# Kernel tuning notes

Hardware: AMD Instinct MI355X
Metric: run time of the kernel (lower is better)

The kernel has to match this reference:

```python
import jax, jax.numpy as jnp
import numpy as np

B, DIM, L, H, W = 4, 128, 256, 8, 8
N = L * H * W
D_INNER, D_STATE, D_CONV, DT_RANK = 128, 8, 4, 8


def _ln(x, w, b, eps=1e-5):
    m = x.mean(-1, keepdims=True)
    v = ((x - m) ** 2).mean(-1, keepdims=True)
    return (x - m) * jax.lax.rsqrt(v + eps) * w + b


def _mamba_fusion(x, z_in, p, i):
    # x, z_in: (B, N, DIM). x drives the SSM; z_in provides the cross-modal gate.
    u = x @ p['Wx'][i]                                    # (B, N, D_INNER)
    z = z_in @ p['Wz'][i]                                 # (B, N, D_INNER)
    # causal depthwise conv1d along tokens, kernel D_CONV (torch pad=k-1 then truncate)
    up = jnp.pad(u, ((0, 0), (D_CONV - 1, 0), (0, 0)))
    w = p['conv_w'][i]                                    # (D_INNER, D_CONV)
    uc = sum(up[:, k:k + u.shape[1], :] * w[:, k] for k in range(D_CONV)) + p['conv_b'][i]
    uc = jax.nn.silu(uc)
    x_dbl = uc @ p['Wxproj'][i]                           # (B, N, DT_RANK + 2*D_STATE)
    dt_r, Bm, Cm = jnp.split(x_dbl, [DT_RANK, DT_RANK + D_STATE], axis=-1)
    dt = jax.nn.softplus(dt_r @ p['Wdt'][i] + p['bdt'][i])  # (B, N, D_INNER)
    A = -jnp.exp(p['A_log'][i])                           # (D_INNER, D_STATE)
    dA = jnp.exp(dt[..., None] * A)                       # (B, N, D_INNER, D_STATE)
    dBu = dt[..., None] * Bm[:, :, None, :] * uc[..., None]

    def step(h, inp):
        dA_t, dBu_t, C_t = inp
        h = dA_t * h + dBu_t                              # (B, D_INNER, D_STATE)
        return h, jnp.einsum('bds,bs->bd', h, C_t)

    h0 = jnp.zeros((u.shape[0], D_INNER, D_STATE), u.dtype)
    _, ys = jax.lax.scan(step, h0, (dA.swapaxes(0, 1), dBu.swapaxes(0, 1), Cm.swapaxes(0, 1)))
    y = ys.swapaxes(0, 1) + p['Dp'][i] * uc
    y = y * jax.nn.silu(z)
    return y @ p['Wout_m'][i] + p['bout_m'][i]


def _cross_block(in0, in1, p, i):
    skip = in0
    a = _ln(in0, p['ln0_w'][i], p['ln0_b'][i])
    b = _ln(in1, p['ln1_w'][i], p['ln1_b'][i])
    return skip + _mamba_fusion(a, b, p, i)


def setup_inputs() -> dict:
    key = jax.random.key(0)
    ks = jax.random.split(key, 16)
    s_in = 1.0 / np.sqrt(DIM)
    s_di = 1.0 / np.sqrt(D_INNER)
    inp = {
        'front': jax.random.normal(ks[0], (B, DIM, L, H, W), jnp.float32),
        'back': jax.random.normal(ks[1], (B, DIM, L, H, W), jnp.float32),
        'ln0_w': jnp.ones((2, DIM), jnp.float32),
        'ln0_b': jnp.zeros((2, DIM), jnp.float32),
        'ln1_w': jnp.ones((2, DIM), jnp.float32),
        'ln1_b': jnp.zeros((2, DIM), jnp.float32),
        'Wx': jax.random.normal(ks[2], (2, DIM, D_INNER), jnp.float32) * s_in,
        'Wz': jax.random.normal(ks[3], (2, DIM, D_INNER), jnp.float32) * s_in,
        'conv_w': jax.random.normal(ks[4], (2, D_INNER, D_CONV), jnp.float32) * 0.5,
        'conv_b': jnp.zeros((2, D_INNER), jnp.float32),
        'Wxproj': jax.random.normal(ks[5], (2, D_INNER, DT_RANK + 2 * D_STATE), jnp.float32) * s_di,
        'Wdt': jax.random.normal(ks[6], (2, DT_RANK, D_INNER), jnp.float32) * (1.0 / np.sqrt(DT_RANK)),
        'bdt': jnp.full((2, D_INNER), -4.6, jnp.float32),  # softplus^-1(~0.01)
        'A_log': jnp.broadcast_to(jnp.log(jnp.arange(1, D_STATE + 1, dtype=jnp.float32)), (2, D_INNER, D_STATE)).copy(),
        'Dp': jnp.ones((2, D_INNER), jnp.float32),
        'Wout_m': jax.random.normal(ks[7], (2, D_INNER, DIM), jnp.float32) * s_di,
        'bout_m': jnp.zeros((2, DIM), jnp.float32),
        'Wout': jax.random.normal(ks[8], (DIM, DIM), jnp.float32) * s_in,
        'bout': jnp.zeros((DIM,), jnp.float32),
    }
    return inp


def reference(front, back, ln0_w, ln0_b, ln1_w, ln1_b, Wx, Wz, conv_w, conv_b,
              Wxproj, Wdt, bdt, A_log, Dp, Wout_m, bout_m, Wout, bout):
    p = dict(ln0_w=ln0_w, ln0_b=ln0_b, ln1_w=ln1_w, ln1_b=ln1_b, Wx=Wx, Wz=Wz,
             conv_w=conv_w, conv_b=conv_b, Wxproj=Wxproj, Wdt=Wdt, bdt=bdt,
             A_log=A_log, Dp=Dp, Wout_m=Wout_m, bout_m=bout_m)
    ff = front.reshape(B, DIM, N).swapaxes(1, 2)          # (B, N, DIM)
    bf = back.reshape(B, DIM, N).swapaxes(1, 2)
    f_fus = _cross_block(ff, bf, p, 0)
    b_fus = _cross_block(bf, ff, p, 1)
    fusion = ((f_fus + b_fus) * 0.5) @ Wout + bout
    return fusion.swapaxes(1, 2).reshape(B, DIM, L, H, W)
```

## Files before the change

### kernel.cpp

```cpp
#include <hip/hip_runtime.h>

#define DEV static __device__ __forceinline__

typedef short s16x8 __attribute__((ext_vector_type(8)));
typedef float f32x4 __attribute__((ext_vector_type(4)));
typedef unsigned short u16;

DEV float b2f(u16 u){ return __uint_as_float(((unsigned int)u) << 16); }
DEV u16 f2b(float f){
  unsigned int x = __float_as_uint(f);
  x += 0x7fffu + ((x >> 16) & 1u);
  return (u16)(x >> 16);
}
DEV float silu_f(float x){ return x * __builtin_amdgcn_rcpf(1.f + __expf(-x)); }
DEV float softplus_f(float x){ return (x > 15.f) ? x : __logf(1.f + __expf(x)); }
DEV bool detf32(const void* lnw){ return *(const unsigned int*)lnw == 0x3F800000u; }
DEV float ldin(const void* p, long long i, bool f){
  return f ? ((const float*)p)[i] : b2f(((const u16*)p)[i]);
}

static constexpr int BATCH = 4;
static constexpr int NSEQ  = 16384;
static constexpr int RTOT  = BATCH * NSEQ;
static constexpr int GCH   = 256;
static constexpr int DIRSZ = BATCH*GCH*128*8;

DEV int swz(int row, int col){ return (row << 7) + (col ^ ((row & 7) << 3)); }

__global__ __launch_bounds__(256) void k_setup(
                        const void* ln0w, const void* ln0b, const void* ln1w, const void* ln1b,
                        const void* Wx, const void* Wz, const void* Wxp, const void* Wdt,
                        const void* bdt, const void* Alog, const void* convw, const void* convb,
                        const void* Dpr, const void* Woutm, const void* boutm,
                        const void* Wout, const void* bout,
                        u16* Wuz, u16* WdtBC, u16* Wcat, u16* WoutT,
                        float* buz, float* bdtf, float* bcat, float* boutf,
                        float* Aexp, float* convwF, float* convbF, float* DpF)
{
  bool f = detf32(ln0w);
  int tid = blockIdx.x * 256 + threadIdx.x;
  int gs  = gridDim.x * 256;
  for (int idx = tid; idx < 2*256*128; idx += gs){
    int d = idx >> 15; int n = (idx >> 7) & 255; int k = idx & 127;
    float wv;
    if (n < 128) wv = ldin(ln0w, d*128+k, f) * ldin(Wx, (long long)(d*128+k)*128 + n, f);
    else         wv = ldin(ln1w, (1-d)*128+k, f) * ldin(Wz, (long long)((1-d)*128+k)*128 + (n-128), f);
    Wuz[idx] = f2b(wv);
  }
  for (int idx = tid; idx < 2*256; idx += gs){
    int d = idx >> 8; int n = idx & 255;
    float s = 0.f;
    if (n < 128){
      for (int k = 0; k < 128; ++k)
        s += ldin(ln0b, d*128+k, f) * ldin(Wx, (long long)(d*128+k)*128 + n, f);
    } else {
      for (int k = 0; k < 128; ++k)
        s += ldin(ln1b, (1-d)*128+k, f) * ldin(Wz, (long long)((1-d)*128+k)*128 + (n-128), f);
    }
    buz[idx] = s;
  }
  for (int idx = tid; idx < 2*128; idx += gs)
    bdtf[idx] = ldin(bdt, idx, f);
  for (int idx = tid; idx < 2*144*128; idx += gs){
    int i = idx / (144*128); int rem = idx % (144*128); int n = rem >> 7; int k = rem & 127;
    if (n < 128){
      float s = 0.f;
      for (int j = 0; j < 8; ++j)
        s += ldin(Wxp, (long long)(i*128+k)*24 + j, f) * ldin(Wdt, (long long)(i*8+j)*128 + n, f);
      WdtBC[idx] = f2b(s);
    } else {
      WdtBC[idx] = f2b(ldin(Wxp, (long long)(i*128+k)*24 + (n - 120), f));
    }
  }
  for (int idx = tid; idx < 128*256; idx += gs){
    int n = idx >> 8; int k = idx & 255;
    Wcat[idx] = f2b(ldin(Woutm, (long long)k*128 + n, f));
  }
  for (int idx = tid; idx < 128*128; idx += gs){
    int n = idx >> 7, k = idx & 127;
    WoutT[idx] = f2b(ldin(Wout, (long long)k*128 + n, f));
  }
  for (int idx = tid; idx < 128; idx += gs){
    bcat[idx]  = ldin(boutm, idx, f) + ldin(boutm, 128 + idx, f);
    boutf[idx] = ldin(bout, idx, f);
  }
  for (int idx = tid; idx < 2*128*8; idx += gs)
    Aexp[idx] = -expf(ldin(Alog, idx, f));
  for (int idx = tid; idx < 2*128*4; idx += gs)
    convwF[idx] = ldin(convw, idx, f);
  for (int idx = tid; idx < 2*128; idx += gs){
    convbF[idx] = ldin(convb, idx, f);
    DpF[idx]   = ldin(Dpr, idx, f);
  }
}

__global__ __launch_bounds__(256) void k_ln(const void* front, const void* back, const void* ln0w,
                                            u16* xf, u16* xb, u16* sfbh)
{
  bool fF = detf32(ln0w);
  __shared__ u16 Af[64][130];
  __shared__ u16 Ab[64][130];
  __shared__ float Mf[64], Rf[64], Mb[64], Rb[64];
  int tid = threadIdx.x;
  long long r0 = (long long)blockIdx.x * 64;
  int b  = (int)(r0 >> 14);
  int n0 = (int)(r0 & 16383);
  if (fF){
    const float* fp = (const float*)front;
    const float* bp = (const float*)back;
    for (int it = 0; it < 8; ++it){
      int d = it*16 + (tid >> 4);
      int t = (tid & 15) * 4;
      long long gi = ((long long)(b*128 + d))*NSEQ + n0 + t;
      float4 vf = *(const float4*)&fp[gi];
      float4 vb = *(const float4*)&bp[gi];
      Af[t+0][d] = f2b(vf.x); Af[t+1][d] = f2b(vf.y);
      Af[t+2][d] = f2b(vf.z); Af[t+3][d] = f2b(vf.w);
      Ab[t+0][d] = f2b(vb.x); Ab[t+1][d] = f2b(vb.y);
      Ab[t+2][d] = f2b(vb.z); Ab[t+3][d] = f2b(vb.w);
    }
  } else {
    const u16* fp = (const u16*)front;
    const u16* bp = (const u16*)back;
    for (int it = 0; it < 4; ++it){
      int d = it*32 + (tid >> 3);
      int t = (tid & 7) * 8;
      long long gi = ((long long)(b*128 + d))*NSEQ + n0 + t;
      uint4 vf = *(const uint4*)&fp[gi];
      uint4 vb = *(const uint4*)&bp[gi];
      Af[t+0][d] = (u16)vf.x; Af[t+1][d] = (u16)(vf.x>>16);
      Af[t+2][d] = (u16)vf.y; Af[t+3][d] = (u16)(vf.y>>16);
      Af[t+4][d] = (u16)vf.z; Af[t+5][d] = (u16)(vf.z>>16);
      Af[t+6][d] = (u16)vf.w; Af[t+7][d] = (u16)(vf.w>>16);
      Ab[t+0][d] = (u16)vb.x; Ab[t+1][d] = (u16)(vb.x>>16);
      Ab[t+2][d] = (u16)vb.y; Ab[t+3][d] = (u16)(vb.y>>16);
      Ab[t+4][d] = (u16)vb.z; Ab[t+5][d] = (u16)(vb.z>>16);
      Ab[t+6][d] = (u16)vb.w; Ab[t+7][d] = (u16)(vb.w>>16);
    }
  }
  __syncthreads();
  {
    int t = tid >> 2, sub = tid & 3;
    float s = 0.f, ss = 0.f, s2 = 0.f, ss2 = 0.f;
    for (int k = 0; k < 32; ++k){
      float v = b2f(Af[t][sub*32 + k]); s  += v; ss  += v*v;
      float w = b2f(Ab[t][sub*32 + k]); s2 += w; ss2 += w*w;
    }
    for (int m = 1; m < 4; m <<= 1){
      s  += __shfl_xor(s,  m, 64); ss  += __shfl_xor(ss,  m, 64);
      s2 += __shfl_xor(s2, m, 64); ss2 += __shfl_xor(ss2, m, 64);
    }
    if (sub == 0){
      float mf = s  * (1.f/128.f); float vf = ss  * (1.f/128.f) - mf*mf;
      Mf[t] = mf; Rf[t] = rsqrtf(vf + 1e-5f);
      float mb = s2 * (1.f/128.f); float vb = ss2 * (1.f/128.f) - mb*mb;
      Mb[t] = mb; Rb[t] = rsqrtf(vb + 1e-5f);
    }
  }
  __syncthreads();
  for (int it = 0; it < 8; ++it){
    int t = it*8 + (tid >> 5);
    int c = (tid & 31) * 4;
    float mf = Mf[t], rf = Rf[t], mb = Mb[t], rb = Rb[t];
    float f0 = b2f(Af[t][c+0]), f1 = b2f(Af[t][c+1]), f2 = b2f(Af[t][c+2]), f3 = b2f(Af[t][c+3]);
    float g0 = b2f(Ab[t][c+0]), g1 = b2f(Ab[t][c+1]), g2 = b2f(Ab[t][c+2]), g3 = b2f(Ab[t][c+3]);
    ushort4 xo, zo, so;
    xo.x = f2b((f0-mf)*rf); xo.y = f2b((f1-mf)*rf); xo.z = f2b((f2-mf)*rf); xo.w = f2b((f3-mf)*rf);
    zo.x = f2b((g0-mb)*rb); zo.y = f2b((g1-mb)*rb); zo.z = f2b((g2-mb)*rb); zo.w = f2b((g3-mb)*rb);
    so.x = f2b(f0+g0); so.y = f2b(f1+g1); so.z = f2b(f2+g2); so.w = f2b(f3+g3);
    long long o = (r0 + t)*128 + c;
    *(ushort4*)&xf[o] = xo;
    *(ushort4*)&xb[o] = zo;
    *(ushort4*)&sfbh[o] = so;
  }
}

__global__ __launch_bounds__(256, 4) void k_guz(const u16* __restrict__ xf,
                                             const u16* __restrict__ xb,
                                             const u16* __restrict__ Wuz,
                                             const float* __restrict__ buz,
                                             u16* __restrict__ u0, u16* __restrict__ u1,
                                             u16* __restrict__ z0, u16* __restrict__ z1)
{
  int dir = blockIdx.y;
  const u16* A = dir ? xb : xf;
  const u16* Wt = Wuz + dir*256*128;
  const float* bias = buz + dir*256;
  u16* outU = dir ? u1 : u0;
  u16* outZ = dir ? z0 : z1;
  __shared__ __align__(16) u16 Wl[256*64];
  __shared__ __align__(16) u16 Al[64*64];
  int tid = threadIdx.x;
  long long r0 = (long long)blockIdx.x * 64;
  int w = tid >> 6, lane = tid & 63;
  int q = lane >> 4, m = lane & 15;
  f32x4 acc[16];
  #pragma unroll
  for (int ct = 0; ct < 16; ++ct) acc[ct] = (f32x4){0.f,0.f,0.f,0.f};
  for (int kp = 0; kp < 2; ++kp){
    if (kp) __syncthreads();
    for (int ci = tid; ci < 256*8; ci += 256){
      int n = ci >> 3, c8 = ci & 7;
      *(uint4*)&Wl[(n << 6) + ((c8 ^ (n & 7)) << 3)] = *(const uint4*)&Wt[n*128 + kp*64 + c8*8];
    }
    for (int ci = tid; ci < 64*8; ci += 256){
      int rl = ci >> 3, c8 = ci & 7;
      *(uint4*)&Al[(rl << 6) + ((c8 ^ (rl & 7)) << 3)] = *(const uint4*)&A[(r0 + rl)*128 + kp*64 + c8*8];
    }
    __syncthreads();
    #pragma unroll
    for (int kt = 0; kt < 2; ++kt){
      int sc = ((kt*4 + q) ^ (m & 7)) << 3;
      s16x8 af = *(const s16x8*)&Al[((w*16 + m) << 6) + sc];
      #pragma unroll
      for (int ct = 0; ct < 16; ++ct){
        s16x8 bf = *(const s16x8*)&Wl[((ct*16 + m) << 6) + sc];
        acc[ct] = __builtin_amdgcn_mfma_f32_16x16x32_bf16(af, bf, acc[ct], 0, 0, 0);
      }
    }
  }
  #pragma unroll
  for (int ct = 0; ct < 16; ++ct){
    int col = ct*16 + m;
    #pragma unroll
    for (int i = 0; i < 4; ++i){
      long long r = r0 + w*16 + q*4 + i;
      float v = acc[ct][i] + bias[col];
      if (col < 128) outU[r*128 + col] = f2b(v);
      else           outZ[r*128 + (col - 128)] = f2b(silu_f(v));
    }
  }
}

__global__ __launch_bounds__(256, 3) void k_cps(const u16* __restrict__ u0p,
                                             const u16* __restrict__ u1p,
                                             const float* __restrict__ convwF,
                                             const float* __restrict__ convbF,
                                             const u16* __restrict__ WdtBC,
                                             const float* __restrict__ bdtf,
                                             const float* __restrict__ Aexp,
                                             u16* __restrict__ uc0p, u16* __restrict__ uc1p,
                                             u16* __restrict__ yg,
                                             float* __restrict__ BCg,
                                             float* __restrict__ P, float* __restrict__ Q)
{
  __shared__ __align__(16) u16 AlF[64*128];
  __shared__ __align__(16) u16 WlF[144*128];
  int dir = blockIdx.y;
  const u16* u = dir ? u1p : u0p;
  u16* ucb = dir ? uc1p : uc0p;
  const u16* Wt = WdtBC + dir*18432;
  const float* bias = bdtf + dir*128;
  u16* dtb = yg + dir*128;
  float* BC = BCg + (long long)dir*RTOT*16;
  int tid = threadIdx.x;
  long long r0 = (long long)blockIdx.x * 64;
  int b  = (int)(r0 >> 14);
  int n0 = (int)(r0 & 16383);
  for (int ci = tid; ci < 144*16; ci += 256){
    int n = ci >> 4, c8 = ci & 15;
    *(uint4*)&WlF[(n << 7) + ((c8 ^ (n & 7)) << 3)] = *(const uint4*)&Wt[n*128 + c8*8];
  }
  {
    int c = tid & 127, h = tid >> 7;
    const float* wp = &convwF[(dir*128 + c)*4];
    float w0 = wp[0], w1 = wp[1], w2 = wp[2], w3 = wp[3];
    float cb = convbF[dir*128 + c];
    int t0 = h*32;
    const u16* up = u + (long long)b*NSEQ*128 + c;
    int nbase = n0 + t0;
    float win0 = (nbase-3 >= 0) ? b2f(up[(long long)(nbase-3)*128]) : 0.f;
    float win1 = (nbase-2 >= 0) ? b2f(up[(long long)(nbase-2)*128]) : 0.f;
    float win2 = (nbase-1 >= 0) ? b2f(up[(long long)(nbase-1)*128]) : 0.f;
    #pragma unroll
    for (int t = 0; t < 32; ++t){
      float cur = b2f(up[(long long)(nbase + t)*128]);
      float a = win0*w0 + win1*w1 + win2*w2 + cur*w3 + cb;
      u16 s = f2b(silu_f(a));
      AlF[swz(t0 + t, c)] = s;
      ucb[(r0 + t0 + t)*128 + c] = s;
      win0 = win1; win1 = win2; win2 = cur;
    }
  }
  __syncthreads();
  int w = tid >> 6, lane = tid & 63;
  int q = lane >> 4, m = lane & 15;
  f32x4 acc[9];
  #pragma unroll
  for (int ct = 0; ct < 9; ++ct) acc[ct] = (f32x4){0.f,0.f,0.f,0.f};
  #pragma unroll
  for (int kt = 0; kt < 4; ++kt){
    int sc = (kt*32 + q*8) ^ ((m & 7) << 3);
    s16x8 af = *(const s16x8*)&AlF[((w*16 + m) << 7) + sc];
    #pragma unroll
    for (int ct = 0; ct < 9; ++ct){
      s16x8 bf = *(const s16x8*)&WlF[((ct*16 + m) << 7) + sc];
      acc[ct] = __builtin_amdgcn_mfma_f32_16x16x32_bf16(af, bf, acc[ct], 0, 0, 0);
    }
  }
  __syncthreads();
  u16* Dl = WlF;
  float* BCl = (float*)&WlF[64*128];
  #pragma unroll
  for (int ct = 0; ct < 9; ++ct){
    int col = ct*16 + m;
    #pragma unroll
    for (int i = 0; i < 4; ++i){
      int rl = w*16 + q*4 + i;
      long long r = r0 + rl;
      float v = acc[ct][i];
      if (col < 128){
        u16 dv = f2b(softplus_f(v + bias[col]));
        dtb[r*256 + col] = dv;
        Dl[swz(rl, col)] = dv;
      } else {
        BC[r*16 + (col - 128)] = v;
        BCl[rl*16 + (col - 128)] = v;
      }
    }
  }
  __syncthreads();
  {
    int c = tid & 127, sh = tid >> 7;
    int g = (int)(r0 & 16383) >> 6;
    int base = sh*4;
    float Ac[4], Pr[4], H[4];
    bool fast = true;
    #pragma unroll
    for (int j = 0; j < 4; ++j){
      Ac[j] = Aexp[(dir*128 + c)*8 + base + j];
      fast = fast && (fabsf(Ac[j] + (float)(base + j + 1)) < 2e-4f);
      H[j] = 0.f;
    }
    float sd = 0.f;
    if (fast){
      if (sh == 0){
        for (int t = 0; t < 64; ++t){
          int ce = swz(t, c);
          float d  = b2f(Dl[ce]);
          float uu = b2f(AlF[ce]);
          float du = d * uu;
          sd += d;
          float E  = __expf(-d);
          float E2 = E*E, E3 = E2*E, E4 = E2*E2;
          float4 bc = *(const float4*)&BCl[t*16];
          H[0] = E *H[0] + du*bc.x;
          H[1] = E2*H[1] + du*bc.y;
          H[2] = E3*H[2] + du*bc.z;
          H[3] = E4*H[3] + du*bc.w;
        }
        float Es = __expf(-sd);
        Pr[0] = Es; Pr[1] = Es*Es; Pr[2] = Pr[1]*Es; Pr[3] = Pr[1]*Pr[1];
      } else {
        for (int t = 0; t < 64; ++t){
          int ce = swz(t, c);
          float d  = b2f(Dl[ce]);
          float uu = b2f(AlF[ce]);
          float du = d * uu;
          sd += d;
          float E  = __expf(-d);
          float E2 = E*E, E4 = E2*E2;
          float E5 = E4*E, E6 = E5*E, E7 = E6*E, E8 = E7*E;
          float4 bc = *(const float4*)&BCl[t*16 + 4];
          H[0] = E5*H[0] + du*bc.x;
          H[1] = E6*H[1] + du*bc.y;
          H[2] = E7*H[2] + du*bc.z;
          H[3] = E8*H[3] + du*bc.w;
        }
        float Es = __expf(-sd);
        float Es2 = Es*Es, Es4 = Es2*Es2;
        Pr[0] = Es4*Es; Pr[1] = Es4*Es2; Pr[2] = Pr[1]*Es; Pr[3] = Es4*Es4;
      }
    } else {
      for (int t = 0; t < 64; ++t){
        int ce = swz(t, c);
        float d  = b2f(Dl[ce]);
        float uu = b2f(AlF[ce]);
        float du = d * uu;
        sd += d;
        #pragma unroll
        for (int j = 0; j < 4; ++j){
          float dA = __expf(d * Ac[j]);
          H[j]  = dA*H[j] + du*BCl[t*16 + base + j];
        }
      }
      #pragma unroll
      for (int j = 0; j < 4; ++j) Pr[j] = __expf(sd * Ac[j]);
    }
    long long o = (long long)dir*DIRSZ + (((long long)b*GCH + g)*128 + c)*8 + base;
    *(float4*)&P[o] = make_float4(Pr[0],Pr[1],Pr[2],Pr[3]);
    *(float4*)&Q[o] = make_float4(H[0],H[1],H[2],H[3]);
  }
}

__global__ __launch_bounds__(64) void k_scan2(const float* __restrict__ P,
                                              const float* __restrict__ Q,
                                              float* __restrict__ hinit)
{
  int idx = blockIdx.x*64 + threadIdx.x;
  int dir = idx >> 12;
  int rem = idx & 4095;
  int b  = rem >> 10;
  int cs = rem & 1023;
  long long base = (long long)dir*DIRSZ + (long long)b*GCH*1024 + cs;
  float h = 0.f;
  for (int g = 0; g < GCH; g += 8){
    long long o = base + (long long)g*1024;
    float p[8], qv[8];
    #pragma unroll
    for (int j = 0; j < 8; ++j){ p[j] = P[o + j*1024]; qv[j] = Q[o + j*1024]; }
    #pragma unroll
    for (int j = 0; j < 8; ++j){
      hinit[o + j*1024] = h;
      h = p[j]*h + qv[j];
    }
  }
}

__global__ __launch_bounds__(256) void k_scan3(const u16* __restrict__ uc0p,
                                               const u16* __restrict__ uc1p,
                                               const float* __restrict__ BCg,
                                               const float* __restrict__ hinit,
                                               const u16* __restrict__ z0p,
                                               const u16* __restrict__ z1p,
                                               const float* __restrict__ DpF,
                                               const float* __restrict__ Aexp,
                                               u16* yg)
{
  __shared__ float Bl[128][8];
  __shared__ float Cl[128][8];
  int dir = blockIdx.y;
  const u16* uc = dir ? uc1p : uc0p;
  const u16* zs = dir ? z1p : z0p;
  const float* BC = BCg + (long long)dir*RTOT*16;
  int tid = threadIdx.x;
  int gp = blockIdx.x & 127;
  int b  = blockIdx.x >> 7;
  long long tokbase = (long long)b*NSEQ + gp*128;
  for (int idx = tid; idx < 128*8; idx += 256){
    int row = idx >> 3, s = idx & 7;
    Bl[row][s] = BC[(tokbase + row)*16 + s];
    Cl[row][s] = BC[(tokbase + row)*16 + 8 + s];
  }
  __syncthreads();
  int c = tid & 127;
  int gh = tid >> 7;
  int g = gp*2 + gh;
  int doff = dir*128;
  float Ac[8], H[8];
  long long ho = (long long)dir*DIRSZ + (((long long)b*GCH + g)*128 + c)*8;
  float4 h0 = *(const float4*)&hinit[ho];
  float4 h1 = *(const float4*)&hinit[ho + 4];
  H[0]=h0.x; H[1]=h0.y; H[2]=h0.z; H[3]=h0.w;
  H[4]=h1.x; H[5]=h1.y; H[6]=h1.z; H[7]=h1.w;
  bool fast = true;
  #pragma unroll
  for (int s = 0; s < 8; ++s){
    Ac[s] = Aexp[(dir*128 + c)*8 + s];
    fast = fast && (fabsf(Ac[s] + (float)(s + 1)) < 2e-4f);
  }
  float dpc = DpF[dir*128 + c];
  long long rbase = (long long)b*NSEQ + g*64;
  if (fast){
    for (int t = 0; t < 64; ++t){
      long long r = rbase + t;
      float d  = b2f(yg[r*256 + doff + c]);
      float uu = b2f(uc[r*128 + c]);
      float du = d * uu;
      int rowl = gh*64 + t;
      float E  = __expf(-d);
      float E2 = E*E, E3 = E2*E, E4 = E2*E2;
      float dA[8] = {E, E2, E3, E4, E4*E, E4*E2, E4*E3, E4*E4};
      float y = 0.f;
      #pragma unroll
      for (int s = 0; s < 8; ++s){
        H[s] = dA[s]*H[s] + du*Bl[rowl][s];
        y += H[s]*Cl[rowl][s];
      }
      float zv = b2f(zs[r*128 + c]);
      yg[r*256 + doff + c] = f2b((y + dpc*uu) * zv);
    }
  } else {
    for (int t = 0; t < 64; ++t){
      long long r = rbase + t;
      float d  = b2f(yg[r*256 + doff + c]);
      float uu = b2f(uc[r*128 + c]);
      float du = d * uu;
      int rowl = gh*64 + t;
      float y = 0.f;
      #pragma unroll
      for (int s = 0; s < 8; ++s){
        float dA = __expf(d * Ac[s]);
        H[s] = dA*H[s] + du*Bl[rowl][s];
        y += H[s]*Cl[rowl][s];
      }
      float zv = b2f(zs[r*128 + c]);
      yg[r*256 + doff + c] = f2b((y + dpc*uu) * zv);
    }
  }
}

__global__ __launch_bounds__(256, 3) void k_tail(const u16* __restrict__ yg,
                                              const u16* __restrict__ Wcat,
                                              const float* __restrict__ bcat,
                                              const u16* __restrict__ sfbh,
                                              const u16* __restrict__ WoutT,
                                              const float* __restrict__ boutf,
                                              void* outp, const void* dflag)
{
  __shared__ u16 Wl[128][136];
  __shared__ u16 Al[64][136];
  int tid = threadIdx.x;
  long long r0 = (long long)blockIdx.x * 64;
  int w = tid >> 6, lane = tid & 63;
  int q = lane >> 4, m = lane & 15;
  f32x4 acc[8];
  #pragma unroll
  for (int ct = 0; ct < 8; ++ct) acc[ct] = (f32x4){0.f,0.f,0.f,0.f};
  for (int kp = 0; kp < 2; ++kp){
    if (kp) __syncthreads();
    for (int ci = tid; ci < 128*16; ci += 256){
      int n = ci >> 4, c8 = ci & 15;
      *(uint4*)&Wl[n][c8*8] = *(const uint4*)&Wcat[n*256 + kp*128 + c8*8];
    }
    for (int ci = tid; ci < 64*16; ci += 256){
      int rl = ci >> 4, c8 = ci & 15;
      *(uint4*)&Al[rl][c8*8] = *(const uint4*)&yg[(r0 + rl)*256 + kp*128 + c8*8];
    }
    __syncthreads();
    #pragma unroll
    for (int kt = 0; kt < 4; ++kt){
      s16x8 af = *(const s16x8*)&Al[w*16 + m][kt*32 + q*8];
      #pragma unroll
      for (int ct = 0; ct < 8; ++ct){
        s16x8 bf = *(const s16x8*)&Wl[ct*16 + m][kt*32 + q*8];
        acc[ct] = __builtin_amdgcn_mfma_f32_16x16x32_bf16(af, bf, acc[ct], 0, 0, 0);
      }
    }
  }
  __syncthreads();
  #pragma unroll
  for (int ct = 0; ct < 8; ++ct){
    int col = ct*16 + m;
    #pragma unroll
    for (int i = 0; i < 4; ++i){
      int rl = w*16 + q*4 + i;
      long long r = r0 + rl;
      Al[rl][col] = f2b(acc[ct][i] + bcat[col] + b2f(sfbh[r*128 + col]));
    }
  }
  for (int ci = tid; ci < 128*16; ci += 256){
    int n = ci >> 4, c8 = ci & 15;
    *(uint4*)&Wl[n][c8*8] = *(const uint4*)&WoutT[n*128 + c8*8];
  }
  __syncthreads();
  f32x4 acc2[8];
  #pragma unroll
  for (int ct = 0; ct < 8; ++ct) acc2[ct] = (f32x4){0.f,0.f,0.f,0.f};
  #pragma unroll
  for (int kt = 0; kt < 4; ++kt){
    s16x8 af = *(const s16x8*)&Al[w*16 + m][kt*32 + q*8];
    #pragma unroll
    for (int ct = 0; ct < 8; ++ct){
      s16x8 bf = *(const s16x8*)&Wl[ct*16 + m][kt*32 + q*8];
      acc2[ct] = __builtin_amdgcn_mfma_f32_16x16x32_bf16(af, bf, acc2[ct], 0, 0, 0);
    }
  }
  __syncthreads();
  u16* Tl = &Wl[0][0];
  #pragma unroll
  for (int ct = 0; ct < 8; ++ct){
    int col = ct*16 + m;
    #pragma unroll
    for (int i = 0; i < 4; ++i){
      int rl = w*16 + q*4 + i;
      Tl[col*68 + rl] = f2b(0.5f*acc2[ct][i] + boutf[col]);
    }
  }
  __syncthreads();
  long long b = r0 >> 14; long long tok0 = r0 & 16383;
  bool fo = detf32(dflag);
  if (fo){
    float* of = (float*)outp;
    for (int idx = tid; idx < 128*16; idx += 256){
      int n = idx >> 4; int t0 = (idx & 15)*4;
      float4 v;
      v.x = b2f(Tl[n*68 + t0+0]); v.y = b2f(Tl[n*68 + t0+1]);
      v.z = b2f(Tl[n*68 + t0+2]); v.w = b2f(Tl[n*68 + t0+3]);
      *(float4*)&of[(((long long)(b*128 + n)) << 14) + tok0 + t0] = v;
    }
  } else {
    u16* ob = (u16*)outp;
    for (int idx = tid; idx < 128*16; idx += 256){
      int n = idx >> 4; int t0 = (idx & 15)*4;
      ushort4 v;
      v.x = Tl[n*68 + t0+0]; v.y = Tl[n*68 + t0+1];
      v.z = Tl[n*68 + t0+2]; v.w = Tl[n*68 + t0+3];
      *(ushort4*)&ob[(((long long)(b*128 + n)) << 14) + tok0 + t0] = v;
    }
  }
}

extern "C" void kernel_launch(void* const* d_in, const int* in_sizes, int n_in,
                              void* d_out, int out_size, void* d_ws, size_t ws_size,
                              hipStream_t stream)
{
  (void)in_sizes; (void)n_in; (void)out_size; (void)ws_size;
  const void* front = d_in[0];
  const void* back  = d_in[1];
  const void* ln0w  = d_in[2];
  const void* ln0b  = d_in[3];
  const void* ln1w  = d_in[4];
  const void* ln1b  = d_in[5];
  const void* Wx    = d_in[6];
  const void* Wz    = d_in[7];
  const void* convw = d_in[8];
  const void* convb = d_in[9];
  const void* Wxp   = d_in[10];
  const void* Wdt   = d_in[11];
  const void* bdt   = d_in[12];
  const void* Alog  = d_in[13];
  const void* Dpr   = d_in[14];
  const void* Woutm = d_in[15];
  const void* boutm = d_in[16];
  const void* Wout  = d_in[17];
  const void* bout  = d_in[18];

  char* p = (char*)d_ws;
  auto alloc = [&](size_t bytes) -> void* {
    void* q = (void*)p; p += (bytes + 255) & ~(size_t)255; return q;
  };
  u16*   xf    = (u16*)  alloc((size_t)RTOT*128*2);
  u16*   xb    = (u16*)  alloc((size_t)RTOT*128*2);
  u16*   sfbh  = (u16*)  alloc((size_t)RTOT*128*2);
  u16*   u0    = (u16*)  alloc((size_t)RTOT*128*2);
  u16*   u1    = (u16*)  alloc((size_t)RTOT*128*2);
  u16*   z0    = (u16*)  alloc((size_t)RTOT*128*2);
  u16*   z1    = (u16*)  alloc((size_t)RTOT*128*2);
  float* BC    = (float*)alloc((size_t)2*RTOT*16*4);
  float* Pb    = (float*)alloc((size_t)2*DIRSZ*4);
  float* Qb    = (float*)alloc((size_t)2*DIRSZ*4);
  float* hin   = (float*)alloc((size_t)2*DIRSZ*4);
  u16*   yg    = (u16*)  alloc((size_t)RTOT*256*2);
  u16*   Wuz   = (u16*)  alloc(2*256*128*2);
  u16*   WdtBC = (u16*)  alloc(2*144*128*2);
  u16*   Wcat  = (u16*)  alloc(128*256*2);
  u16*   WoutT = (u16*)  alloc(128*128*2);
  float* buz   = (float*)alloc(2*256*4);
  float* bdtf  = (float*)alloc(2*128*4);
  float* bcat  = (float*)alloc(128*4);
  float* boutf = (float*)alloc(128*4);
  float* Aexp  = (float*)alloc(2*128*8*4);
  float* convwF= (float*)alloc(2*128*4*4);
  float* convbF= (float*)alloc(2*128*4);
  float* DpF   = (float*)alloc(2*128*4);

  k_setup<<<128,256,0,stream>>>(ln0w,ln0b,ln1w,ln1b,Wx,Wz,Wxp,Wdt,bdt,Alog,convw,convb,Dpr,
                                Woutm,boutm,Wout,bout,
                                Wuz,WdtBC,Wcat,WoutT,buz,bdtf,bcat,boutf,Aexp,
                                convwF,convbF,DpF);
  k_ln<<<RTOT/64,256,0,stream>>>(front,back,ln0w,xf,xb,sfbh);

  dim3 g2(RTOT/64, 2);
  k_guz<<<g2,256,0,stream>>>(xf, xb, Wuz, buz, u0, u1, z0, z1);
  k_cps<<<g2,256,0,stream>>>(u0, u1, convwF, convbF, WdtBC, bdtf, Aexp,
                             xf, xb, yg, BC, Pb, Qb);
  k_scan2<<<128,64,0,stream>>>(Pb, Qb, hin);
  dim3 g3(BATCH*GCH/2, 2);
  k_scan3<<<g3,256,0,stream>>>(xf, xb, BC, hin, z0, z1, DpF, Aexp, yg);
  k_tail<<<RTOT/64,256,0,stream>>>(yg, Wcat, bcat, sfbh, WoutT, boutf, d_out, ln0w);
}
```

Measured before the change: 326.5 us.

## Fuse layernorm into the u/z projection GEMM kernel

Merges the layernorm kernel with the u/z input-projection GEMM so that normalized activations stay in shared memory and feed the MFMA directly. This removes the write and re-read of the two normalized activation buffers in global memory and one kernel launch. In exchange, each block now processes both directions and reloads weight chunks in 64-column pieces, taking A fragments with unaligned 32-bit LDS reads from the padded transpose buffer. The grid is also halved, so each block does more serial work. The freed workspace buffers are renamed and reused for the conv outputs.

```diff
diff --git a/kernel.cpp b/kernel.cpp
--- a/kernel.cpp
+++ b/kernel.cpp
@@ -5,6 +5,7 @@
 typedef short s16x8 __attribute__((ext_vector_type(8)));
 typedef float f32x4 __attribute__((ext_vector_type(4)));
 typedef unsigned short u16;
+typedef unsigned int u32;
 
 DEV float b2f(u16 u){ return __uint_as_float(((unsigned int)u) << 16); }
 DEV u16 f2b(float f){
@@ -94,12 +95,18 @@
   }
 }
 
-__global__ __launch_bounds__(256) void k_ln(const void* front, const void* back, const void* ln0w,
-                                            u16* xf, u16* xb, u16* sfbh)
+__global__ __launch_bounds__(256, 3) void k_lnguz(const void* front, const void* back,
+                                                  const void* ln0w,
+                                                  const u16* __restrict__ Wuz,
+                                                  const float* __restrict__ buz,
+                                                  u16* __restrict__ sfbh,
+                                                  u16* __restrict__ u0, u16* __restrict__ u1,
+                                                  u16* __restrict__ z0, u16* __restrict__ z1)
 {
   bool fF = detf32(ln0w);
-  __shared__ u16 Af[64][130];
-  __shared__ u16 Ab[64][130];
+  __shared__ u16 Tf[64][130];
+  __shared__ u16 Tb[64][130];
+  __shared__ __align__(16) u16 Wl[64*128];
   __shared__ float Mf[64], Rf[64], Mb[64], Rb[64];
   int tid = threadIdx.x;
   long long r0 = (long long)blockIdx.x * 64;
@@ -114,10 +121,10 @@
       long long gi = ((long long)(b*128 + d))*NSEQ + n0 + t;
       float4 vf = *(const float4*)&fp[gi];
       float4 vb = *(const float4*)&bp[gi];
-      Af[t+0][d] = f2b(vf.x); Af[t+1][d] = f2b(vf.y);
-      Af[t+2][d] = f2b(vf.z); Af[t+3][d] = f2b(vf.w);
-      Ab[t+0][d] = f2b(vb.x); Ab[t+1][d] = f2b(vb.y);
-      Ab[t+2][d] = f2b(vb.z); Ab[t+3][d] = f2b(vb.w);
+      Tf[t+0][d] = f2b(vf.x); Tf[t+1][d] = f2b(vf.y);
+      Tf[t+2][d] = f2b(vf.z); Tf[t+3][d] = f2b(vf.w);
+      Tb[t+0][d] = f2b(vb.x); Tb[t+1][d] = f2b(vb.y);
+      Tb[t+2][d] = f2b(vb.z); Tb[t+3][d] = f2b(vb.w);
     }
   } else {
     const u16* fp = (const u16*)front;
@@ -128,14 +135,14 @@
       long long gi = ((long long)(b*128 + d))*NSEQ + n0 + t;
       uint4 vf = *(const uint4*)&fp[gi];
       uint4 vb = *(const uint4*)&bp[gi];
-      Af[t+0][d] = (u16)vf.x; Af[t+1][d] = (u16)(vf.x>>16);
-      Af[t+2][d] = (u16)vf.y; Af[t+3][d] = (u16)(vf.y>>16);
-      Af[t+4][d] = (u16)vf.z; Af[t+5][d] = (u16)(vf.z>>16);
-      Af[t+6][d] = (u16)vf.w; Af[t+7][d] = (u16)(vf.w>>16);
-      Ab[t+0][d] = (u16)vb.x; Ab[t+1][d] = (u16)(vb.x>>16);
-      Ab[t+2][d] = (u16)vb.y; Ab[t+3][d] = (u16)(vb.y>>16);
-      Ab[t+4][d] = (u16)vb.z; Ab[t+5][d] = (u16)(vb.z>>16);
-      Ab[t+6][d] = (u16)vb.w; Ab[t+7][d] = (u16)(vb.w>>16);
+      Tf[t+0][d] = (u16)vf.x; Tf[t+1][d] = (u16)(vf.x>>16);
+      Tf[t+2][d] = (u16)vf.y; Tf[t+3][d] = (u16)(vf.y>>16);
+      Tf[t+4][d] = (u16)vf.z; Tf[t+5][d] = (u16)(vf.z>>16);
+      Tf[t+6][d] = (u16)vf.w; Tf[t+7][d] = (u16)(vf.w>>16);
+      Tb[t+0][d] = (u16)vb.x; Tb[t+1][d] = (u16)(vb.x>>16);
+      Tb[t+2][d] = (u16)vb.y; Tb[t+3][d] = (u16)(vb.y>>16);
+      Tb[t+4][d] = (u16)vb.z; Tb[t+5][d] = (u16)(vb.z>>16);
+      Tb[t+6][d] = (u16)vb.w; Tb[t+7][d] = (u16)(vb.w>>16);
     }
   }
   __syncthreads();
@@ -143,8 +150,8 @@
     int t = tid >> 2, sub = tid & 3;
     float s = 0.f, ss = 0.f, s2 = 0.f, ss2 = 0.f;
     for (int k = 0; k < 32; ++k){
-      float v = b2f(Af[t][sub*32 + k]); s  += v; ss  += v*v;
-      float w = b2f(Ab[t][sub*32 + k]); s2 += w; ss2 += w*w;
+      float v = b2f(Tf[t][sub*32 + k]); s  += v; ss  += v*v;
+      float w = b2f(Tb[t][sub*32 + k]); s2 += w; ss2 += w*w;
     }
     for (int m = 1; m < 4; m <<= 1){
       s  += __shfl_xor(s,  m, 64); ss  += __shfl_xor(ss,  m, 64);
@@ -162,72 +169,61 @@
     int t = it*8 + (tid >> 5);
     int c = (tid & 31) * 4;
     float mf = Mf[t], rf = Rf[t], mb = Mb[t], rb = Rb[t];
-    float f0 = b2f(Af[t][c+0]), f1 = b2f(Af[t][c+1]), f2 = b2f(Af[t][c+2]), f3 = b2f(Af[t][c+3]);
-    float g0 = b2f(Ab[t][c+0]), g1 = b2f(Ab[t][c+1]), g2 = b2f(Ab[t][c+2]), g3 = b2f(Ab[t][c+3]);
-    ushort4 xo, zo, so;
-    xo.x = f2b((f0-mf)*rf); xo.y = f2b((f1-mf)*rf); xo.z = f2b((f2-mf)*rf); xo.w = f2b((f3-mf)*rf);
-    zo.x = f2b((g0-mb)*rb); zo.y = f2b((g1-mb)*rb); zo.z = f2b((g2-mb)*rb); zo.w = f2b((g3-mb)*rb);
+    float f0 = b2f(Tf[t][c+0]), f1 = b2f(Tf[t][c+1]), f2 = b2f(Tf[t][c+2]), f3 = b2f(Tf[t][c+3]);
+    float g0 = b2f(Tb[t][c+0]), g1 = b2f(Tb[t][c+1]), g2 = b2f(Tb[t][c+2]), g3 = b2f(Tb[t][c+3]);
+    ushort4 so;
     so.x = f2b(f0+g0); so.y = f2b(f1+g1); so.z = f2b(f2+g2); so.w = f2b(f3+g3);
-    long long o = (r0 + t)*128 + c;
-    *(ushort4*)&xf[o] = xo;
-    *(ushort4*)&xb[o] = zo;
-    *(ushort4*)&sfbh[o] = so;
-  }
-}
-
-__global__ __launch_bounds__(256, 4) void k_guz(const u16* __restrict__ xf,
-                                             const u16* __restrict__ xb,
-                                             const u16* __restrict__ Wuz,
-                                             const float* __restrict__ buz,
-                                             u16* __restrict__ u0, u16* __restrict__ u1,
-                                             u16* __restrict__ z0, u16* __restrict__ z1)
-{
-  int dir = blockIdx.y;
-  const u16* A = dir ? xb : xf;
-  const u16* Wt = Wuz + dir*256*128;
-  const float* bias = buz + dir*256;
-  u16* outU = dir ? u1 : u0;
-  u16* outZ = dir ? z0 : z1;
-  __shared__ __align__(16) u16 Wl[256*64];
-  __shared__ __align__(16) u16 Al[64*64];
-  int tid = threadIdx.x;
-  long long r0 = (long long)blockIdx.x * 64;
+    *(ushort4*)&sfbh[(r0 + t)*128 + c] = so;
+    Tf[t][c+0] = f2b((f0-mf)*rf); Tf[t][c+1] = f2b((f1-mf)*rf);
+    Tf[t][c+2] = f2b((f2-mf)*rf); Tf[t][c+3] = f2b((f3-mf)*rf);
+    Tb[t][c+0] = f2b((g0-mb)*rb); Tb[t][c+1] = f2b((g1-mb)*rb);
+    Tb[t][c+2] = f2b((g2-mb)*rb); Tb[t][c+3] = f2b((g3-mb)*rb);
+  }
+  __syncthreads();
   int w = tid >> 6, lane = tid & 63;
   int q = lane >> 4, m = lane & 15;
-  f32x4 acc[16];
-  #pragma unroll
-  for (int ct = 0; ct < 16; ++ct) acc[ct] = (f32x4){0.f,0.f,0.f,0.f};
-  for (int kp = 0; kp < 2; ++kp){
-    if (kp) __syncthreads();
-    for (int ci = tid; ci < 256*8; ci += 256){
-      int n = ci >> 3, c8 = ci & 7;
-      *(uint4*)&Wl[(n << 6) + ((c8 ^ (n & 7)) << 3)] = *(const uint4*)&Wt[n*128 + kp*64 + c8*8];
-    }
-    for (int ci = tid; ci < 64*8; ci += 256){
-      int rl = ci >> 3, c8 = ci & 7;
-      *(uint4*)&Al[(rl << 6) + ((c8 ^ (rl & 7)) << 3)] = *(const uint4*)&A[(r0 + rl)*128 + kp*64 + c8*8];
-    }
-    __syncthreads();
-    #pragma unroll
-    for (int kt = 0; kt < 2; ++kt){
-      int sc = ((kt*4 + q) ^ (m & 7)) << 3;
-      s16x8 af = *(const s16x8*)&Al[((w*16 + m) << 6) + sc];
+  for (int dir = 0; dir < 2; ++dir){
+    const u16* At = dir ? &Tb[0][0] : &Tf[0][0];
+    const u16* Wt = Wuz + dir*256*128;
+    const float* bias = buz + dir*256;
+    u16* outU = dir ? u1 : u0;
+    u16* outZ = dir ? z0 : z1;
+    for (int ch = 0; ch < 4; ++ch){
+      for (int ci = tid; ci < 64*16; ci += 256){
+        int n = ci >> 4, c8 = ci & 15;
+        *(uint4*)&Wl[(n << 7) + ((c8 ^ (n & 7)) << 3)] = *(const uint4*)&Wt[(ch*64 + n)*128 + c8*8];
+      }
+      __syncthreads();
+      f32x4 acc[4];
       #pragma unroll
-      for (int ct = 0; ct < 16; ++ct){
-        s16x8 bf = *(const s16x8*)&Wl[((ct*16 + m) << 6) + sc];
-        acc[ct] = __builtin_amdgcn_mfma_f32_16x16x32_bf16(af, bf, acc[ct], 0, 0, 0);
-      }
-    }
-  }
-  #pragma unroll
-  for (int ct = 0; ct < 16; ++ct){
-    int col = ct*16 + m;
-    #pragma unroll
-    for (int i = 0; i < 4; ++i){
-      long long r = r0 + w*16 + q*4 + i;
-      float v = acc[ct][i] + bias[col];
-      if (col < 128) outU[r*128 + col] = f2b(v);
-      else           outZ[r*128 + (col - 128)] = f2b(silu_f(v));
+      for (int ct = 0; ct < 4; ++ct) acc[ct] = (f32x4){0.f,0.f,0.f,0.f};
+      #pragma unroll
+      for (int kt = 0; kt < 4; ++kt){
+        const u16* ap = At + (w*16 + m)*130 + kt*32 + q*8;
+        union { u32 w4[4]; s16x8 v; } au;
+        au.w4[0] = *(const u32*)&ap[0];
+        au.w4[1] = *(const u32*)&ap[2];
+        au.w4[2] = *(const u32*)&ap[4];
+        au.w4[3] = *(const u32*)&ap[6];
+        int sc = (kt*32 + q*8) ^ ((m & 7) << 3);
+        #pragma unroll
+        for (int ct = 0; ct < 4; ++ct){
+          s16x8 bf = *(const s16x8*)&Wl[((ct*16 + m) << 7) + sc];
+          acc[ct] = __builtin_amdgcn_mfma_f32_16x16x32_bf16(au.v, bf, acc[ct], 0, 0, 0);
+        }
+      }
+      #pragma unroll
+      for (int ct = 0; ct < 4; ++ct){
+        int col = ch*64 + ct*16 + m;
+        #pragma unroll
+        for (int i = 0; i < 4; ++i){
+          long long r = r0 + w*16 + q*4 + i;
+          float v = acc[ct][i] + bias[col];
+          if (col < 128) outU[r*128 + col] = f2b(v);
+          else           outZ[r*128 + (col - 128)] = f2b(silu_f(v));
+        }
+      }
+      __syncthreads();
     }
   }
 }
@@ -630,8 +626,8 @@
   auto alloc = [&](size_t bytes) -> void* {
     void* q = (void*)p; p += (bytes + 255) & ~(size_t)255; return q;
   };
-  u16*   xf    = (u16*)  alloc((size_t)RTOT*128*2);
-  u16*   xb    = (u16*)  alloc((size_t)RTOT*128*2);
+  u16*   uc0   = (u16*)  alloc((size_t)RTOT*128*2);
+  u16*   uc1   = (u16*)  alloc((size_t)RTOT*128*2);
   u16*   sfbh  = (u16*)  alloc((size_t)RTOT*128*2);
   u16*   u0    = (u16*)  alloc((size_t)RTOT*128*2);
   u16*   u1    = (u16*)  alloc((size_t)RTOT*128*2);
@@ -659,14 +655,13 @@
                                 Woutm,boutm,Wout,bout,
                                 Wuz,WdtBC,Wcat,WoutT,buz,bdtf,bcat,boutf,Aexp,
                                 convwF,convbF,DpF);
-  k_ln<<<RTOT/64,256,0,stream>>>(front,back,ln0w,xf,xb,sfbh);
-
+  k_lnguz<<<RTOT/64,256,0,stream>>>(front, back, ln0w, Wuz, buz, sfbh,
+                                    u0, u1, z0, z1);
   dim3 g2(RTOT/64, 2);
-  k_guz<<<g2,256,0,stream>>>(xf, xb, Wuz, buz, u0, u1, z0, z1);
   k_cps<<<g2,256,0,stream>>>(u0, u1, convwF, convbF, WdtBC, bdtf, Aexp,
-                             xf, xb, yg, BC, Pb, Qb);
+                             uc0, uc1, yg, BC, Pb, Qb);
   k_scan2<<<128,64,0,stream>>>(Pb, Qb, hin);
   dim3 g3(BATCH*GCH/2, 2);
-  k_scan3<<<g3,256,0,stream>>>(xf, xb, BC, hin, z0, z1, DpF, Aexp, yg);
+  k_scan3<<<g3,256,0,stream>>>(uc0, uc1, BC, hin, z0, z1, DpF, Aexp, yg);
   k_tail<<<RTOT/64,256,0,stream>>>(yg, Wcat, bcat, sfbh, WoutT, boutf, d_out, ln0w);
 }
```

Measured after the change: 312.1 us. 1.05x faster.
